# Performance work log

Measured on AMD Instinct MI355X. Metric: run time of the kernel, lower is better.

The kernel has to match this reference:

```python
import jax, jax.numpy as jnp
import numpy as np

B, LQ, D, H, L, P, DFF = 16, 1024, 256, 8, 4, 4, 1024
SHAPES = ((64, 64), (32, 32), (16, 16), (8, 8))  # (H_l, W_l) per level
LV = sum(h * w for h, w in SHAPES)  # 5440
DH = D // H
EPS = 1e-5


def layer_norm(x, g, b):
    m = jnp.mean(x, -1, keepdims=True)
    v = jnp.mean((x - m) ** 2, -1, keepdims=True)
    return (x - m) * jax.lax.rsqrt(v + EPS) * g + b


def mha(q_in, k_in, v_in, w, b, ow, ob):
    # torch nn.MultiheadAttention with packed in_proj [3D, D]
    q = (q_in @ w[:D].T + b[:D]).reshape(B, LQ, H, DH)
    k = (k_in @ w[D:2 * D].T + b[D:2 * D]).reshape(B, LQ, H, DH)
    v = (v_in @ w[2 * D:].T + b[2 * D:]).reshape(B, LQ, H, DH)
    a = jax.nn.softmax(jnp.einsum('bqhd,bkhd->bhqk', q, k) * (1.0 / np.sqrt(DH)), -1)
    o = jnp.einsum('bhqk,bkhd->bqhd', a, v).reshape(B, LQ, D)
    return o @ ow.T + ob


def ms_deform_attn(q, ref, src, value_w, value_b, off_w, off_b, attw_w, attw_b, outp_w, outp_b):
    # value: [B, H, LV, DH]
    value = (src @ value_w.T + value_b).reshape(B, LV, H, DH).transpose(0, 2, 1, 3)
    off = (q @ off_w.T + off_b).reshape(B, LQ, H, L, P, 2)
    attw = jax.nn.softmax((q @ attw_w.T + attw_b).reshape(B, LQ, H, L * P), -1).reshape(B, LQ, H, L, P)
    # offset normalizer = (W_l, H_l) matching (x, y) order of reference points
    normalizer = jnp.array([[w, h] for h, w in SHAPES], jnp.float32)
    loc = ref[:, :, None, :, None, :] + off / normalizer[None, None, None, :, None, :]  # [B,LQ,H,L,P,2]
    out = jnp.zeros((B, LQ, H, DH), jnp.float32)
    start = 0
    for l, (hl, wl) in enumerate(SHAPES):
        v = value[:, :, start:start + hl * wl]  # [B,H,N_l,DH]
        start += hl * wl
        # grid_sample semantics, align_corners=False, padding zeros
        x = loc[:, :, :, l, :, 0] * wl - 0.5  # [B,LQ,H,P]
        y = loc[:, :, :, l, :, 1] * hl - 0.5
        x0 = jnp.floor(x); y0 = jnp.floor(y)
        lx = (x - x0).transpose(0, 2, 1, 3)[..., None]  # [B,H,LQ,P,1]
        ly = (y - y0).transpose(0, 2, 1, 3)[..., None]
        x0i = x0.astype(jnp.int32); y0i = y0.astype(jnp.int32)

        def gather(xi, yi):
            valid = ((xi >= 0) & (xi < wl) & (yi >= 0) & (yi < hl)).astype(jnp.float32)
            idx = jnp.clip(yi, 0, hl - 1) * wl + jnp.clip(xi, 0, wl - 1)  # [B,LQ,H,P]
            idx2 = idx.transpose(0, 2, 1, 3).reshape(B, H, LQ * P)
            g = jnp.take_along_axis(v, jnp.broadcast_to(idx2[..., None], (B, H, LQ * P, DH)), axis=2)
            return g.reshape(B, H, LQ, P, DH) * valid.transpose(0, 2, 1, 3)[..., None]

        g00 = gather(x0i, y0i); g01 = gather(x0i + 1, y0i)
        g10 = gather(x0i, y0i + 1); g11 = gather(x0i + 1, y0i + 1)
        sampled = (g00 * (1 - lx) * (1 - ly) + g01 * lx * (1 - ly)
                   + g10 * (1 - lx) * ly + g11 * lx * ly)  # [B,H,LQ,P,DH]
        out = out + jnp.einsum('bhqpd,bqhp->bqhd', sampled, attw[:, :, :, l])
    return out.reshape(B, LQ, D) @ outp_w.T + outp_b


def setup_inputs() -> dict:
    key = jax.random.key(0)
    ks = jax.random.split(key, 16)
    s = 0.02
    inp = {}
    inp['tgt'] = jax.random.normal(ks[0], (B, LQ, D), jnp.float32)
    inp['query_pos'] = jax.random.normal(ks[1], (B, LQ, D), jnp.float32)
    inp['reference_points'] = jax.random.uniform(ks[2], (B, LQ, L, 2), jnp.float32)
    inp['src'] = jax.random.normal(ks[3], (B, LV, D), jnp.float32)
    # self-attention (MHA)
    inp['in_proj_w'] = jax.random.normal(ks[4], (3 * D, D), jnp.float32) * s
    inp['in_proj_b'] = jnp.zeros((3 * D,), jnp.float32)
    inp['out_proj_w'] = jax.random.normal(ks[5], (D, D), jnp.float32) * s
    inp['out_proj_b'] = jnp.zeros((D,), jnp.float32)
    inp['norm2_g'] = jnp.ones((D,), jnp.float32); inp['norm2_b'] = jnp.zeros((D,), jnp.float32)
    # MSDeformAttn
    inp['value_w'] = jax.random.normal(ks[6], (D, D), jnp.float32) * s
    inp['value_b'] = jnp.zeros((D,), jnp.float32)
    inp['off_w'] = jax.random.normal(ks[7], (H * L * P * 2, D), jnp.float32) * s
    inp['off_b'] = jax.random.normal(ks[8], (H * L * P * 2,), jnp.float32) * 0.5
    inp['attw_w'] = jax.random.normal(ks[9], (H * L * P, D), jnp.float32) * s
    inp['attw_b'] = jnp.zeros((H * L * P,), jnp.float32)
    inp['outp_w'] = jax.random.normal(ks[10], (D, D), jnp.float32) * s
    inp['outp_b'] = jnp.zeros((D,), jnp.float32)
    inp['norm1_g'] = jnp.ones((D,), jnp.float32); inp['norm1_b'] = jnp.zeros((D,), jnp.float32)
    # FFN
    inp['lin1_w'] = jax.random.normal(ks[11], (DFF, D), jnp.float32) * s
    inp['lin1_b'] = jnp.zeros((DFF,), jnp.float32)
    inp['lin2_w'] = jax.random.normal(ks[12], (D, DFF), jnp.float32) * s
    inp['lin2_b'] = jnp.zeros((D,), jnp.float32)
    inp['norm3_g'] = jnp.ones((D,), jnp.float32); inp['norm3_b'] = jnp.zeros((D,), jnp.float32)
    inp['src_spatial_shapes'] = jnp.array(SHAPES, jnp.int32)
    inp['level_start_index'] = jnp.array(np.concatenate([[0], np.cumsum([h * w for h, w in SHAPES[:-1]])]), jnp.int32)
    return inp


def reference(tgt, query_pos, reference_points, src,
              in_proj_w, in_proj_b, out_proj_w, out_proj_b, norm2_g, norm2_b,
              value_w, value_b, off_w, off_b, attw_w, attw_b, outp_w, outp_b,
              norm1_g, norm1_b, lin1_w, lin1_b, lin2_w, lin2_b, norm3_g, norm3_b,
              src_spatial_shapes, level_start_index):
    # dropout=0 (eval mode)
    q = tgt + query_pos
    tgt2 = mha(q, q, tgt, in_proj_w, in_proj_b, out_proj_w, out_proj_b)
    tgt = layer_norm(tgt + tgt2, norm2_g, norm2_b)
    tgt2 = ms_deform_attn(tgt + query_pos, reference_points, src,
                          value_w, value_b, off_w, off_b, attw_w, attw_b, outp_w, outp_b)
    tgt = layer_norm(tgt + tgt2, norm1_g, norm1_b)
    t2 = jax.nn.relu(tgt @ lin1_w.T + lin1_b) @ lin2_w.T + lin2_b
    return layer_norm(tgt + t2, norm3_g, norm3_b)
```

## Files before the change

kernel.cpp:

```cpp
#include <hip/hip_runtime.h>
#include <math.h>

typedef short s16x8 __attribute__((ext_vector_type(8)));
typedef float f32x4 __attribute__((ext_vector_type(4)));
typedef unsigned short u16;
typedef unsigned short u16x4 __attribute__((ext_vector_type(4)));

constexpr int cB    = 16;
constexpr int cLQ   = 1024;
constexpr int cD    = 256;
constexpr int cH    = 8;
constexpr int cLVTOT= 5440;
constexpr int cNTOK = cB * cLQ;
constexpr int cNV   = cB * cLVTOT;

__device__ __forceinline__ u16 f2b(float f) {
    __bf16 h = (__bf16)f;
    u16 u;
    __builtin_memcpy(&u, &h, 2);
    return u;
}
__device__ __forceinline__ float bl(unsigned x) {
    return __uint_as_float(x << 16);
}

__global__ __launch_bounds__(256) void prep_src_kernel(const float4* __restrict__ t,
                                                       const float4* __restrict__ q,
                                                       u16x4* __restrict__ tb,
                                                       u16x4* __restrict__ qb,
                                                       const float4* __restrict__ src,
                                                       u16x4* __restrict__ srcb) {
    int bid = blockIdx.x;
    if (bid < 4096) {
        int i = bid * 256 + threadIdx.x;
        float4 a = t[i], b = q[i];
        tb[i] = (u16x4){ f2b(a.x), f2b(a.y), f2b(a.z), f2b(a.w) };
        qb[i] = (u16x4){ f2b(a.x + b.x), f2b(a.y + b.y), f2b(a.z + b.z), f2b(a.w + b.w) };
    } else {
        int i = (bid - 4096) * 256 + threadIdx.x;
        float4 v = src[i];
        srcb[i] = (u16x4){ f2b(v.x), f2b(v.y), f2b(v.z), f2b(v.w) };
    }
}

struct WArgs { const float4* src[8]; };
__global__ __launch_bounds__(256) void cvtw_kernel(WArgs a, u16x4* __restrict__ out,
                                                   const float* __restrict__ off_b,
                                                   const float* __restrict__ attw_b,
                                                   float* __restrict__ biasoa) {
    int i = blockIdx.x * 256 + threadIdx.x;
    if (i >= 253952) {
        int t = threadIdx.x;
        biasoa[t] = off_b[t];
        if (t < 128) biasoa[256 + t] = attw_b[t];
        return;
    }
    int s, off;
    if (i < 98304) {
        if (i < 65536) { if (i < 49152) { s = 0; off = i; } else { s = 1; off = i - 49152; } }
        else           { if (i < 81920) { s = 2; off = i - 65536; } else { s = 3; off = i - 81920; } }
    } else {
        if (i < 122880){ if (i < 106496){ s = 4; off = i - 98304; } else { s = 5; off = i - 106496; } }
        else           { if (i < 188416){ s = 6; off = i - 122880; } else { s = 7; off = i - 188416; } }
    }
    float4 v = a.src[s][off];
    out[i] = (u16x4){ f2b(v.x), f2b(v.y), f2b(v.z), f2b(v.w) };
}

__global__ __launch_bounds__(256) void gemm_qkv(const u16* __restrict__ A0,
                                                const u16* __restrict__ A1,
                                                const u16* __restrict__ Wt,
                                                const float* __restrict__ bias,
                                                u16* __restrict__ QKb,
                                                u16* __restrict__ Vtg) {
    __shared__ u16 As[128 * 32];
    __shared__ u16 Bs[128 * 32];
    const int K = 256;
    int tid = threadIdx.x;
    int bm = blockIdx.x * 128, bn = blockIdx.y * 128;
    const u16* A = (blockIdx.y < 4) ? A0 : A1;
    int w = tid >> 6, lane = tid & 63, quad = lane >> 4, l15 = lane & 15;
    int wm = (w & 1) * 64, wn = (w >> 1) * 64;
    int r0 = tid >> 2;
    int c0 = ((tid & 3) ^ ((tid >> 3) & 3)) * 8;
    const u16* ga0 = A  + (size_t)(bm + r0) * K + c0;
    const u16* ga1 = ga0 + (size_t)64 * K;
    const u16* gb0 = Wt + (size_t)(bn + r0) * K + c0;
    const u16* gb1 = gb0 + (size_t)64 * K;
    int abk = (quad ^ ((l15 >> 1) & 3)) * 8;
    f32x4 acc[16];
#pragma unroll
    for (int i = 0; i < 16; ++i) acc[i] = (f32x4){0.f, 0.f, 0.f, 0.f};
    s16x8 ra0 = *(const s16x8*)ga0, ra1 = *(const s16x8*)ga1;
    s16x8 rb0 = *(const s16x8*)gb0, rb1 = *(const s16x8*)gb1;
#pragma unroll 2
    for (int i = 0; i < 8; ++i) {
        *(s16x8*)&As[tid * 8]        = ra0;
        *(s16x8*)&As[2048 + tid * 8] = ra1;
        *(s16x8*)&Bs[tid * 8]        = rb0;
        *(s16x8*)&Bs[2048 + tid * 8] = rb1;
        __syncthreads();
        if (i < 7) {
            int k1 = (i + 1) << 5;
            ra0 = *(const s16x8*)(ga0 + k1); ra1 = *(const s16x8*)(ga1 + k1);
            rb0 = *(const s16x8*)(gb0 + k1); rb1 = *(const s16x8*)(gb1 + k1);
        }
        s16x8 af[4], bf[4];
#pragma unroll
        for (int mt = 0; mt < 4; ++mt) af[mt] = *(const s16x8*)&As[(wm + mt * 16 + l15) * 32 + abk];
#pragma unroll
        for (int nt = 0; nt < 4; ++nt) bf[nt] = *(const s16x8*)&Bs[(wn + nt * 16 + l15) * 32 + abk];
#pragma unroll
        for (int mt = 0; mt < 4; ++mt)
#pragma unroll
            for (int nt = 0; nt < 4; ++nt)
                acc[mt * 4 + nt] = __builtin_amdgcn_mfma_f32_16x16x32_bf16(af[mt], bf[nt], acc[mt * 4 + nt], 0, 0, 0);
        __syncthreads();
    }
    float bs[4];
#pragma unroll
    for (int nt = 0; nt < 4; ++nt) bs[nt] = bias[bn + wn + nt * 16 + l15];
    if (bn < 512) {
        float qs = (bn + wn < 256) ? 0.25506734f : 1.0f;
#pragma unroll
        for (int mt = 0; mt < 4; ++mt) {
            int m = bm + wm + mt * 16 + quad * 4;
#pragma unroll
            for (int nt = 0; nt < 4; ++nt) {
                int n = bn + wn + nt * 16 + l15;
#pragma unroll
                for (int r = 0; r < 4; ++r)
                    QKb[(size_t)(m + r) * 512 + n] = f2b((acc[mt * 4 + nt][r] + bs[nt]) * qs);
            }
        }
    } else {
#pragma unroll
        for (int mt = 0; mt < 4; ++mt) {
            int m = bm + wm + mt * 16 + quad * 4;
            int b = m >> 10, t = m & 1023;
#pragma unroll
            for (int nt = 0; nt < 4; ++nt) {
                int nv = bn + wn + nt * 16 + l15 - 512;
                int h = nv >> 5, dh = nv & 31;
                u16x4 o;
#pragma unroll
                for (int r = 0; r < 4; ++r) o[r] = f2b(acc[mt * 4 + nt][r] + bs[nt]);
                *(u16x4*)(Vtg + (((size_t)(b * 8 + h) * 32 + dh) << 10) + t) = o;
            }
        }
    }
}

template <int RELU, int OUTBF>
__global__ __launch_bounds__(256) void gemm128(const u16* __restrict__ A,
                                               const u16* __restrict__ Wt,
                                               const float* __restrict__ bias,
                                               float* __restrict__ Cf,
                                               u16* __restrict__ Cb,
                                               int M, int N, int K) {
    __shared__ u16 As[128 * 32];
    __shared__ u16 Bs[128 * 32];
    int tid = threadIdx.x;
    int bm = blockIdx.x * 128, bn = blockIdx.y * 128;
    int w = tid >> 6, lane = tid & 63, quad = lane >> 4, l15 = lane & 15;
    int wm = (w & 1) * 64, wn = (w >> 1) * 64;
    int r0 = tid >> 2;
    int c0 = ((tid & 3) ^ ((tid >> 3) & 3)) * 8;
    const u16* ga0 = A  + (size_t)(bm + r0) * K + c0;
    const u16* ga1 = ga0 + (size_t)64 * K;
    const u16* gb0 = Wt + (size_t)(bn + r0) * K + c0;
    const u16* gb1 = gb0 + (size_t)64 * K;
    int abk = (quad ^ ((l15 >> 1) & 3)) * 8;
    f32x4 acc[16];
#pragma unroll
    for (int i = 0; i < 16; ++i) acc[i] = (f32x4){0.f, 0.f, 0.f, 0.f};
    s16x8 ra0 = *(const s16x8*)ga0, ra1 = *(const s16x8*)ga1;
    s16x8 rb0 = *(const s16x8*)gb0, rb1 = *(const s16x8*)gb1;
    int nk = K >> 5;
#pragma unroll 2
    for (int i = 0; i < nk; ++i) {
        *(s16x8*)&As[tid * 8]        = ra0;
        *(s16x8*)&As[2048 + tid * 8] = ra1;
        *(s16x8*)&Bs[tid * 8]        = rb0;
        *(s16x8*)&Bs[2048 + tid * 8] = rb1;
        __syncthreads();
        if (i + 1 < nk) {
            int k1 = (i + 1) << 5;
            ra0 = *(const s16x8*)(ga0 + k1); ra1 = *(const s16x8*)(ga1 + k1);
            rb0 = *(const s16x8*)(gb0 + k1); rb1 = *(const s16x8*)(gb1 + k1);
        }
        s16x8 af[4], bf[4];
#pragma unroll
        for (int mt = 0; mt < 4; ++mt) af[mt] = *(const s16x8*)&As[(wm + mt * 16 + l15) * 32 + abk];
#pragma unroll
        for (int nt = 0; nt < 4; ++nt) bf[nt] = *(const s16x8*)&Bs[(wn + nt * 16 + l15) * 32 + abk];
#pragma unroll
        for (int mt = 0; mt < 4; ++mt)
#pragma unroll
            for (int nt = 0; nt < 4; ++nt)
                acc[mt * 4 + nt] = __builtin_amdgcn_mfma_f32_16x16x32_bf16(af[mt], bf[nt], acc[mt * 4 + nt], 0, 0, 0);
        __syncthreads();
    }
    float bs[4];
#pragma unroll
    for (int nt = 0; nt < 4; ++nt) bs[nt] = bias[bn + wn + nt * 16 + l15];
#pragma unroll
    for (int mt = 0; mt < 4; ++mt) {
        int m = bm + wm + mt * 16 + quad * 4;
#pragma unroll
        for (int nt = 0; nt < 4; ++nt) {
            int n = bn + wn + nt * 16 + l15;
#pragma unroll
            for (int r = 0; r < 4; ++r) {
                float v = acc[mt * 4 + nt][r] + bs[nt];
                if (RELU) v = fmaxf(v, 0.f);
                if (OUTBF) Cb[(size_t)(m + r) * N + n] = f2b(v);
                else       Cf[(size_t)(m + r) * N + n] = v;
            }
        }
    }
}

template <int RELU, int OUTBF>
__global__ __launch_bounds__(256) void gemm64(const u16* __restrict__ A,
                                              const u16* __restrict__ Wt,
                                              const float* __restrict__ bias,
                                              float* __restrict__ Cf,
                                              u16* __restrict__ Cb,
                                              int M, int N, int K) {
    __shared__ u16 As[64 * 32];
    __shared__ u16 Bs[128 * 32];
    int tid = threadIdx.x;
    int bm = blockIdx.x * 64, bn = blockIdx.y * 128;
    int w = tid >> 6, lane = tid & 63, quad = lane >> 4, l15 = lane & 15;
    int wn = w * 32;
    int r0 = tid >> 2;
    int c0 = ((tid & 3) ^ ((tid >> 3) & 3)) * 8;
    const u16* ga0 = A  + (size_t)(bm + r0) * K + c0;
    const u16* gb0 = Wt + (size_t)(bn + r0) * K + c0;
    const u16* gb1 = gb0 + (size_t)64 * K;
    int abk = (quad ^ ((l15 >> 1) & 3)) * 8;
    f32x4 acc[8];
#pragma unroll
    for (int i = 0; i < 8; ++i) acc[i] = (f32x4){0.f, 0.f, 0.f, 0.f};
    s16x8 ra0 = *(const s16x8*)ga0;
    s16x8 rb0 = *(const s16x8*)gb0, rb1 = *(const s16x8*)gb1;
    int nk = K >> 5;
#pragma unroll 2
    for (int i = 0; i < nk; ++i) {
        *(s16x8*)&As[tid * 8]        = ra0;
        *(s16x8*)&Bs[tid * 8]        = rb0;
        *(s16x8*)&Bs[2048 + tid * 8] = rb1;
        __syncthreads();
        if (i + 1 < nk) {
            int k1 = (i + 1) << 5;
            ra0 = *(const s16x8*)(ga0 + k1);
            rb0 = *(const s16x8*)(gb0 + k1); rb1 = *(const s16x8*)(gb1 + k1);
        }
        s16x8 af[4], bf[2];
#pragma unroll
        for (int mt = 0; mt < 4; ++mt) af[mt] = *(const s16x8*)&As[(mt * 16 + l15) * 32 + abk];
#pragma unroll
        for (int nt = 0; nt < 2; ++nt) bf[nt] = *(const s16x8*)&Bs[(wn + nt * 16 + l15) * 32 + abk];
#pragma unroll
        for (int mt = 0; mt < 4; ++mt)
#pragma unroll
            for (int nt = 0; nt < 2; ++nt)
                acc[mt * 2 + nt] = __builtin_amdgcn_mfma_f32_16x16x32_bf16(af[mt], bf[nt], acc[mt * 2 + nt], 0, 0, 0);
        __syncthreads();
    }
    float bs[2];
#pragma unroll
    for (int nt = 0; nt < 2; ++nt) bs[nt] = bias[bn + wn + nt * 16 + l15];
#pragma unroll
    for (int mt = 0; mt < 4; ++mt) {
        int m = bm + mt * 16 + quad * 4;
#pragma unroll
        for (int nt = 0; nt < 2; ++nt) {
            int n = bn + wn + nt * 16 + l15;
#pragma unroll
            for (int r = 0; r < 4; ++r) {
                float v = acc[mt * 2 + nt][r] + bs[nt];
                if (RELU) v = fmaxf(v, 0.f);
                if (OUTBF) Cb[(size_t)(m + r) * N + n] = f2b(v);
                else       Cf[(size_t)(m + r) * N + n] = v;
            }
        }
    }
}

__global__ __launch_bounds__(256) void attn_mfma(const u16* __restrict__ QK,
                                                 const u16* __restrict__ Vt,
                                                 u16* __restrict__ O) {
    __shared__ u16 Ks[64 * 40];
    __shared__ u16 Vs[32 * 72];
    __shared__ u16 Ps[4][16 * 72];
    int tid = threadIdx.x, w = tid >> 6, lane = tid & 63, quad = lane >> 4, l15 = lane & 15;
    int qt = blockIdx.x & 15, bh = blockIdx.x >> 4;
    int h = bh & 7, b = bh >> 3;
    int qbase = qt * 64 + w * 16;
    s16x8 qf = *(const s16x8*)(QK + (size_t)(b * cLQ + qbase + l15) * 512 + h * 32 + quad * 8);
    f32x4 o0 = {0.f,0.f,0.f,0.f}, o1 = {0.f,0.f,0.f,0.f};
    float lsum = 0.f;
    int skey = tid >> 2, sdh = (tid & 3) * 8;
    int vdh = tid >> 3, vkc = (tid & 7) * 8;
    size_t kgbase = (size_t)(b * cLQ) * 512 + 256 + h * 32;
    size_t vgbase = (size_t)bh * 32 * cLQ;
    s16x8 kreg = *(const s16x8*)(QK + kgbase + (size_t)skey * 512 + sdh);
    s16x8 vreg = *(const s16x8*)(Vt + vgbase + (size_t)vdh * cLQ + vkc);
    for (int kt = 0; kt < cLQ; kt += 64) {
        __syncthreads();
        *(s16x8*)&Ks[skey * 40 + sdh] = kreg;
        *(s16x8*)&Vs[vdh * 72 + vkc]  = vreg;
        if (kt + 64 < cLQ) {
            kreg = *(const s16x8*)(QK + kgbase + (size_t)(kt + 64 + skey) * 512 + sdh);
            vreg = *(const s16x8*)(Vt + vgbase + (size_t)vdh * cLQ + kt + 64 + vkc);
        }
        __syncthreads();
#pragma unroll
        for (int t = 0; t < 4; ++t) {
            s16x8 kf = *(const s16x8*)&Ks[(t * 16 + l15) * 40 + quad * 8];
            f32x4 z = {0.f,0.f,0.f,0.f};
            f32x4 sc = __builtin_amdgcn_mfma_f32_16x16x32_bf16(kf, qf, z, 0, 0, 0);
            u16x4 pb;
#pragma unroll
            for (int r = 0; r < 4; ++r) {
                float p = exp2f(sc[r]);
                lsum += p;
                pb[r] = f2b(p);
            }
            *(u16x4*)&Ps[w][l15 * 72 + t * 16 + quad * 4] = pb;
        }
#pragma unroll
        for (int ks = 0; ks < 2; ++ks) {
            s16x8 pa  = *(const s16x8*)&Ps[w][l15 * 72 + ks * 32 + quad * 8];
            s16x8 vb0 = *(const s16x8*)&Vs[l15 * 72 + ks * 32 + quad * 8];
            s16x8 vb1 = *(const s16x8*)&Vs[(l15 + 16) * 72 + ks * 32 + quad * 8];
            o0 = __builtin_amdgcn_mfma_f32_16x16x32_bf16(pa, vb0, o0, 0, 0, 0);
            o1 = __builtin_amdgcn_mfma_f32_16x16x32_bf16(pa, vb1, o1, 0, 0, 0);
        }
    }
    lsum += __shfl_xor(lsum, 16);
    lsum += __shfl_xor(lsum, 32);
#pragma unroll
    for (int r = 0; r < 4; ++r) {
        float inv = 1.0f / __shfl(lsum, quad * 4 + r);
        int q = qbase + quad * 4 + r;
        size_t ob = (size_t)(b * cLQ + q) * cD + h * 32;
        O[ob + l15]      = f2b(o0[r] * inv);
        O[ob + 16 + l15] = f2b(o1[r] * inv);
    }
}

template <int WB, int QP>
__global__ __launch_bounds__(256) void add_ln_kernel(const float* __restrict__ X,
                                                     const float* __restrict__ R,
                                                     const float* __restrict__ g,
                                                     const float* __restrict__ bt,
                                                     const float* __restrict__ qp,
                                                     float* __restrict__ out,
                                                     u16* __restrict__ outb) {
    int wave = threadIdx.x / 64;
    int lane = threadIdx.x % 64;
    int row = blockIdx.x * 4 + wave;
    const float* x = X + (size_t)row * cD;
    const float* r = R + (size_t)row * cD;
    float4 xv = *(const float4*)(x + lane * 4);
    float4 rv = *(const float4*)(r + lane * 4);
    float v0 = xv.x + rv.x, v1 = xv.y + rv.y, v2 = xv.z + rv.z, v3 = xv.w + rv.w;
    float s = v0 + v1 + v2 + v3;
    float s2 = v0 * v0 + v1 * v1 + v2 * v2 + v3 * v3;
#pragma unroll
    for (int off = 32; off > 0; off >>= 1) {
        s += __shfl_xor(s, off);
        s2 += __shfl_xor(s2, off);
    }
    float mean = s * (1.0f / 256.0f);
    float var = s2 * (1.0f / 256.0f) - mean * mean;
    float rstd = rsqrtf(var + 1e-5f);
    float4 gv = *(const float4*)(g + lane * 4);
    float4 bv = *(const float4*)(bt + lane * 4);
    float4 o;
    o.x = (v0 - mean) * rstd * gv.x + bv.x;
    o.y = (v1 - mean) * rstd * gv.y + bv.y;
    o.z = (v2 - mean) * rstd * gv.z + bv.z;
    o.w = (v3 - mean) * rstd * gv.w + bv.w;
    *(float4*)(out + (size_t)row * cD + lane * 4) = o;
    if (WB) {
        u16x4 ob = { f2b(o.x), f2b(o.y), f2b(o.z), f2b(o.w) };
        *(u16x4*)(outb + (size_t)row * cD + lane * 4) = ob;
    }
    if (QP) {
        float4 qv = *(const float4*)(qp + (size_t)row * cD + lane * 4);
        u16x4 ob = { f2b(o.x + qv.x), f2b(o.y + qv.y), f2b(o.z + qv.z), f2b(o.w + qv.w) };
        *(u16x4*)(outb + (size_t)row * cD + lane * 4) = ob;
    }
}

__global__ __launch_bounds__(256) void deform_kernel(const u16* __restrict__ value,
                                                     const float* __restrict__ oa,
                                                     const float* __restrict__ refp,
                                                     u16* __restrict__ out) {
    int t = blockIdx.x * 32 + (threadIdx.x >> 3);
    int dq = threadIdx.x & 7;
    int h = t & 7;
    int bq = t >> 3;
    int b = bq >> 10;
    const float* al = oa + (size_t)bq * 384 + 256 + h * 16;
    float wv[16];
    float mx = -1e30f;
#pragma unroll
    for (int i = 0; i < 16; ++i) { wv[i] = al[i]; mx = fmaxf(mx, wv[i]); }
    float sum = 0.f;
#pragma unroll
    for (int i = 0; i < 16; ++i) { wv[i] = __expf(wv[i] - mx); sum += wv[i]; }
    float inv = 1.f / sum;
    const float* off = oa + (size_t)bq * 384 + h * 32;
    const float* rp = refp + (size_t)bq * 8;
    const u16* vb = value + ((size_t)b * cLVTOT) * 256 + h * 32 + dq * 4;
    const int starts[4] = {0, 4096, 5120, 5376};
    const int dims[4] = {64, 32, 16, 8};
    float a0 = 0.f, a1 = 0.f, a2 = 0.f, a3 = 0.f;
#pragma unroll
    for (int l = 0; l < 4; ++l) {
        int hl = dims[l], wl = dims[l];
        float rx = rp[l * 2 + 0], ry = rp[l * 2 + 1];
#pragma unroll
        for (int p = 0; p < 4; ++p) {
            float ox = off[(l * 4 + p) * 2 + 0];
            float oy = off[(l * 4 + p) * 2 + 1];
            float x = rx * (float)wl + ox - 0.5f;
            float y = ry * (float)hl + oy - 0.5f;
            float x0f = floorf(x), y0f = floorf(y);
            float lx = x - x0f, ly = y - y0f;
            int x0 = (int)x0f, y0 = (int)y0f;
            float aw = wv[l * 4 + p] * inv;
            float cw[4] = {(1.f - lx) * (1.f - ly), lx * (1.f - ly),
                           (1.f - lx) * ly, lx * ly};
            int xs[4] = {x0, x0 + 1, x0, x0 + 1};
            int ys[4] = {y0, y0, y0 + 1, y0 + 1};
#pragma unroll
            for (int c = 0; c < 4; ++c) {
                int xi = xs[c], yi = ys[c];
                bool valid = (xi >= 0) && (xi < wl) && (yi >= 0) && (yi < hl);
                int xc = min(max(xi, 0), wl - 1);
                int yc = min(max(yi, 0), hl - 1);
                int idx = starts[l] + yc * wl + xc;
                float wgt = valid ? aw * cw[c] : 0.f;
                unsigned long long u = *(const unsigned long long*)(vb + (size_t)idx * 256);
                a0 += wgt * bl((unsigned)(u & 0xffffull));
                a1 += wgt * bl((unsigned)((u >> 16) & 0xffffull));
                a2 += wgt * bl((unsigned)((u >> 32) & 0xffffull));
                a3 += wgt * bl((unsigned)(u >> 48));
            }
        }
    }
    u16x4 o = { f2b(a0), f2b(a1), f2b(a2), f2b(a3) };
    *(u16x4*)(out + (size_t)bq * 256 + h * 32 + dq * 4) = o;
}

extern "C" void kernel_launch(void* const* d_in, const int* in_sizes, int n_in,
                              void* d_out, int out_size, void* d_ws, size_t ws_size,
                              hipStream_t stream) {
    const float* tgt        = (const float*)d_in[0];
    const float* query_pos  = (const float*)d_in[1];
    const float* refp       = (const float*)d_in[2];
    const float* src        = (const float*)d_in[3];
    const float* in_proj_w  = (const float*)d_in[4];
    const float* in_proj_b  = (const float*)d_in[5];
    const float* out_proj_b = (const float*)d_in[7];
    const float* norm2_g    = (const float*)d_in[8];
    const float* norm2_b    = (const float*)d_in[9];
    const float* value_b    = (const float*)d_in[11];
    const float* off_b      = (const float*)d_in[13];
    const float* attw_b     = (const float*)d_in[15];
    const float* outp_b     = (const float*)d_in[17];
    const float* norm1_g    = (const float*)d_in[18];
    const float* norm1_b    = (const float*)d_in[19];
    const float* lin1_b     = (const float*)d_in[21];
    const float* lin2_b     = (const float*)d_in[23];
    const float* norm3_g    = (const float*)d_in[24];
    const float* norm3_b    = (const float*)d_in[25];

    char* W = (char*)d_ws;
    const size_t S84 = 8388608;
    u16*   tgtb  = (u16*)(W + 0);
    u16*   q2b   = (u16*)(W + 0);
    u16*   qb    = (u16*)(W + 1 * S84);
    u16*   QKb   = (u16*)(W + 2 * S84);
    u16*   dtb   = (u16*)(W + 2 * S84);
    u16*   x2b   = (u16*)(W + 3 * S84);
    float* ffn2f = (float*)(W + 4 * S84);
    u16*   aob   = (u16*)(W + 5 * S84);
    float* oaf   = (float*)(W + 5 * S84);
    u16*   Vtg   = (u16*)(W + 6 * S84);
    float* t2f   = (float*)(W + 6 * S84);
    float* x1f   = (float*)(W + 8 * S84);
    float* x2f   = (float*)(W + 10 * S84);
    u16*   srcb  = (u16*)(W + 12 * S84);
    u16*   ffn1b = (u16*)(W + 12 * S84);
    u16*   valb  = (u16*)(W + 12 * S84 + 44564480);
    char*  wbase = W + 12 * S84 + 2 * 44564480;
    u16* wb_in   = (u16*)(wbase + 0);
    u16* wb_out  = (u16*)(wbase + 393216);
    u16* wb_val  = (u16*)(wbase + 524288);
    u16* wb_off  = (u16*)(wbase + 655360);
    u16* wb_outp = (u16*)(wbase + 851968);
    u16* wb_lin1 = (u16*)(wbase + 983040);
    u16* wb_lin2 = (u16*)(wbase + 1507328);
    float* biasoa= (float*)(wbase + 2031616);
    float* out = (float*)d_out;

    dim3 blk(256);

    prep_src_kernel<<<dim3(25856), blk, 0, stream>>>((const float4*)tgt, (const float4*)query_pos,
                                                     (u16x4*)tgtb, (u16x4*)qb,
                                                     (const float4*)src, (u16x4*)srcb);
    WArgs wa;
    wa.src[0] = (const float4*)in_proj_w;  wa.src[1] = (const float4*)d_in[6];
    wa.src[2] = (const float4*)d_in[10];   wa.src[3] = (const float4*)d_in[12];
    wa.src[4] = (const float4*)d_in[14];   wa.src[5] = (const float4*)d_in[16];
    wa.src[6] = (const float4*)d_in[20];   wa.src[7] = (const float4*)d_in[22];
    cvtw_kernel<<<dim3(993), blk, 0, stream>>>(wa, (u16x4*)wb_in, off_b, attw_b, biasoa);

    gemm_qkv<<<dim3(128, 6), blk, 0, stream>>>(qb, tgtb, wb_in, in_proj_b, QKb, Vtg);
    attn_mfma<<<dim3(cB * cH * 16), blk, 0, stream>>>(QKb, Vtg, aob);
    gemm64<0, 0><<<dim3(256, 2), blk, 0, stream>>>(aob, wb_out, out_proj_b, t2f, nullptr, cNTOK, 256, 256);
    add_ln_kernel<0, 1><<<dim3(4096), blk, 0, stream>>>(tgt, t2f, norm2_g, norm2_b, query_pos, x1f, q2b);

    gemm128<0, 1><<<dim3(680, 2), blk, 0, stream>>>(srcb, wb_val, value_b, nullptr, valb, cNV, 256, 256);
    gemm64<0, 0><<<dim3(256, 3), blk, 0, stream>>>(q2b, wb_off, biasoa, oaf, nullptr, cNTOK, 384, 256);
    deform_kernel<<<dim3(4096), blk, 0, stream>>>(valb, oaf, refp, dtb);
    gemm64<0, 0><<<dim3(256, 2), blk, 0, stream>>>(dtb, wb_outp, outp_b, t2f, nullptr, cNTOK, 256, 256);
    add_ln_kernel<1, 0><<<dim3(4096), blk, 0, stream>>>(x1f, t2f, norm1_g, norm1_b, nullptr, x2f, x2b);

    gemm128<1, 1><<<dim3(128, 8), blk, 0, stream>>>(x2b, wb_lin1, lin1_b, nullptr, ffn1b, cNTOK, 1024, 256);
    gemm64<0, 0><<<dim3(256, 2), blk, 0, stream>>>(ffn1b, wb_lin2, lin2_b, ffn2f, nullptr, cNTOK, 256, 1024);
    add_ln_kernel<0, 0><<<dim3(4096), blk, 0, stream>>>(x2f, ffn2f, norm3_g, norm3_b, nullptr, out, nullptr);
}
```

Baseline: 443.2 us.

## Co-schedule value projection GEMM with self-attention in one interleaved launch

```diff
diff --git a/kernel.cpp b/kernel.cpp
--- a/kernel.cpp
+++ b/kernel.cpp
@@ -289,29 +289,102 @@
     }
 }
 
-__global__ __launch_bounds__(256) void attn_mfma(const u16* __restrict__ QK,
-                                                 const u16* __restrict__ Vt,
-                                                 u16* __restrict__ O) {
-    __shared__ u16 Ks[64 * 40];
-    __shared__ u16 Vs[32 * 72];
-    __shared__ u16 Ps[4][16 * 72];
-    int tid = threadIdx.x, w = tid >> 6, lane = tid & 63, quad = lane >> 4, l15 = lane & 15;
-    int qt = blockIdx.x & 15, bh = blockIdx.x >> 4;
+__global__ __launch_bounds__(256) void attn_val(const u16* __restrict__ QK,
+                                                const u16* __restrict__ Vt,
+                                                u16* __restrict__ O,
+                                                const u16* __restrict__ Av,
+                                                const u16* __restrict__ Wv,
+                                                const float* __restrict__ bv,
+                                                u16* __restrict__ Cv) {
+    __shared__ __align__(16) u16 smem[8192];
+    int bid = blockIdx.x;
+    int tid = threadIdx.x;
+    int w = tid >> 6, lane = tid & 63, quad = lane >> 4, l15 = lane & 15;
+    int isg, id;
+    if (bid < 2720) { isg = !(bid & 1); id = bid >> 1; }
+    else            { isg = 0;          id = 1360 + (bid - 2720); }
+    if (isg) {
+        u16* As = smem;
+        u16* Bs = smem + 4096;
+        int bm = (id % 680) * 128, bn = (id / 680) * 128;
+        int wm = (w & 1) * 64, wn = (w >> 1) * 64;
+        int r0 = tid >> 2;
+        int c0 = ((tid & 3) ^ ((tid >> 3) & 3)) * 8;
+        const u16* ga0 = Av + (size_t)(bm + r0) * 256 + c0;
+        const u16* ga1 = ga0 + (size_t)64 * 256;
+        const u16* gb0 = Wv + (size_t)(bn + r0) * 256 + c0;
+        const u16* gb1 = gb0 + (size_t)64 * 256;
+        int abk = (quad ^ ((l15 >> 1) & 3)) * 8;
+        f32x4 acc[16];
+#pragma unroll
+        for (int i = 0; i < 16; ++i) acc[i] = (f32x4){0.f, 0.f, 0.f, 0.f};
+        s16x8 ra0 = *(const s16x8*)ga0, ra1 = *(const s16x8*)ga1;
+        s16x8 rb0 = *(const s16x8*)gb0, rb1 = *(const s16x8*)gb1;
+#pragma unroll 2
+        for (int i = 0; i < 8; ++i) {
+            *(s16x8*)&As[tid * 8]        = ra0;
+            *(s16x8*)&As[2048 + tid * 8] = ra1;
+            *(s16x8*)&Bs[tid * 8]        = rb0;
+            *(s16x8*)&Bs[2048 + tid * 8] = rb1;
+            __syncthreads();
+            if (i < 7) {
+                int k1 = (i + 1) << 5;
+                ra0 = *(const s16x8*)(ga0 + k1); ra1 = *(const s16x8*)(ga1 + k1);
+                rb0 = *(const s16x8*)(gb0 + k1); rb1 = *(const s16x8*)(gb1 + k1);
+            }
+            s16x8 af[4], bf[4];
+#pragma unroll
+            for (int mt = 0; mt < 4; ++mt) af[mt] = *(const s16x8*)&As[(wm + mt * 16 + l15) * 32 + abk];
+#pragma unroll
+            for (int nt = 0; nt < 4; ++nt) bf[nt] = *(const s16x8*)&Bs[(wn + nt * 16 + l15) * 32 + abk];
+#pragma unroll
+            for (int mt = 0; mt < 4; ++mt)
+#pragma unroll
+                for (int nt = 0; nt < 4; ++nt)
+                    acc[mt * 4 + nt] = __builtin_amdgcn_mfma_f32_16x16x32_bf16(af[mt], bf[nt], acc[mt * 4 + nt], 0, 0, 0);
+            __syncthreads();
+        }
+        float bs[4];
+#pragma unroll
+        for (int nt = 0; nt < 4; ++nt) bs[nt] = bv[bn + wn + nt * 16 + l15];
+#pragma unroll
+        for (int mt = 0; mt < 4; ++mt) {
+            int m = bm + wm + mt * 16 + quad * 4;
+#pragma unroll
+            for (int nt = 0; nt < 4; ++nt) {
+                int n = bn + wn + nt * 16 + l15;
+#pragma unroll
+                for (int r = 0; r < 4; ++r)
+                    Cv[(size_t)(m + r) * 256 + n] = f2b(acc[mt * 4 + nt][r] + bs[nt]);
+            }
+        }
+        return;
+    }
+    u16* Ks  = smem;
+    u16* Vs  = smem + 2048;
+    u16* Psw = smem + 4096 + w * 1024;
+    int qt = id & 15, bh = id >> 4;
     int h = bh & 7, b = bh >> 3;
     int qbase = qt * 64 + w * 16;
     s16x8 qf = *(const s16x8*)(QK + (size_t)(b * cLQ + qbase + l15) * 512 + h * 32 + quad * 8);
-    f32x4 o0 = {0.f,0.f,0.f,0.f}, o1 = {0.f,0.f,0.f,0.f};
-    float lsum = 0.f;
-    int skey = tid >> 2, sdh = (tid & 3) * 8;
-    int vdh = tid >> 3, vkc = (tid & 7) * 8;
+    f32x4 o0 = {0.f,0.f,0.f,0.f}, o1 = {0.f,0.f,0.f,0.f}, o2 = {0.f,0.f,0.f,0.f};
+    int skey = tid >> 2, kchunk = tid & 3;
+    int ks_off = skey * 32 + ((kchunk ^ ((skey >> 1) & 3)) * 8);
+    int sdh = kchunk * 8;
+    int vdh = tid >> 3, vchunk = tid & 7;
+    int vs_off = vdh * 64 + ((vchunk ^ (vdh & 7)) * 8);
+    int vkc = vchunk * 8;
+    int ksw = (l15 >> 1) & 3;
+    int vsw = l15 & 7;
     size_t kgbase = (size_t)(b * cLQ) * 512 + 256 + h * 32;
     size_t vgbase = (size_t)bh * 32 * cLQ;
     s16x8 kreg = *(const s16x8*)(QK + kgbase + (size_t)skey * 512 + sdh);
     s16x8 vreg = *(const s16x8*)(Vt + vgbase + (size_t)vdh * cLQ + vkc);
+    const s16x8 ones = {16256,16256,16256,16256,16256,16256,16256,16256};
     for (int kt = 0; kt < cLQ; kt += 64) {
         __syncthreads();
-        *(s16x8*)&Ks[skey * 40 + sdh] = kreg;
-        *(s16x8*)&Vs[vdh * 72 + vkc]  = vreg;
+        *(s16x8*)&Ks[ks_off] = kreg;
+        *(s16x8*)&Vs[vs_off] = vreg;
         if (kt + 64 < cLQ) {
             kreg = *(const s16x8*)(QK + kgbase + (size_t)(kt + 64 + skey) * 512 + sdh);
             vreg = *(const s16x8*)(Vt + vgbase + (size_t)vdh * cLQ + kt + 64 + vkc);
@@ -319,32 +392,28 @@
         __syncthreads();
 #pragma unroll
         for (int t = 0; t < 4; ++t) {
-            s16x8 kf = *(const s16x8*)&Ks[(t * 16 + l15) * 40 + quad * 8];
+            s16x8 kf = *(const s16x8*)&Ks[(t * 16 + l15) * 32 + (quad ^ ksw) * 8];
             f32x4 z = {0.f,0.f,0.f,0.f};
             f32x4 sc = __builtin_amdgcn_mfma_f32_16x16x32_bf16(kf, qf, z, 0, 0, 0);
             u16x4 pb;
 #pragma unroll
-            for (int r = 0; r < 4; ++r) {
-                float p = exp2f(sc[r]);
-                lsum += p;
-                pb[r] = f2b(p);
-            }
-            *(u16x4*)&Ps[w][l15 * 72 + t * 16 + quad * 4] = pb;
+            for (int r = 0; r < 4; ++r) pb[r] = f2b(exp2f(sc[r]));
+            *(u16x4*)&Psw[l15 * 64 + (((t * 2 + (quad >> 1)) ^ vsw) * 8) + (quad & 1) * 4] = pb;
         }
 #pragma unroll
         for (int ks = 0; ks < 2; ++ks) {
-            s16x8 pa  = *(const s16x8*)&Ps[w][l15 * 72 + ks * 32 + quad * 8];
-            s16x8 vb0 = *(const s16x8*)&Vs[l15 * 72 + ks * 32 + quad * 8];
-            s16x8 vb1 = *(const s16x8*)&Vs[(l15 + 16) * 72 + ks * 32 + quad * 8];
+            int coff = ((ks * 4 + quad) ^ vsw) * 8;
+            s16x8 pa  = *(const s16x8*)&Psw[l15 * 64 + coff];
+            s16x8 vb0 = *(const s16x8*)&Vs[l15 * 64 + coff];
+            s16x8 vb1 = *(const s16x8*)&Vs[(l15 + 16) * 64 + coff];
             o0 = __builtin_amdgcn_mfma_f32_16x16x32_bf16(pa, vb0, o0, 0, 0, 0);
             o1 = __builtin_amdgcn_mfma_f32_16x16x32_bf16(pa, vb1, o1, 0, 0, 0);
-        }
-    }
-    lsum += __shfl_xor(lsum, 16);
-    lsum += __shfl_xor(lsum, 32);
+            o2 = __builtin_amdgcn_mfma_f32_16x16x32_bf16(pa, ones, o2, 0, 0, 0);
+        }
+    }
 #pragma unroll
     for (int r = 0; r < 4; ++r) {
-        float inv = 1.0f / __shfl(lsum, quad * 4 + r);
+        float inv = 1.0f / o2[r];
         int q = qbase + quad * 4 + r;
         size_t ob = (size_t)(b * cLQ + q) * cD + h * 32;
         O[ob + l15]      = f2b(o0[r] * inv);
@@ -524,11 +593,10 @@
     cvtw_kernel<<<dim3(993), blk, 0, stream>>>(wa, (u16x4*)wb_in, off_b, attw_b, biasoa);
 
     gemm_qkv<<<dim3(128, 6), blk, 0, stream>>>(qb, tgtb, wb_in, in_proj_b, QKb, Vtg);
-    attn_mfma<<<dim3(cB * cH * 16), blk, 0, stream>>>(QKb, Vtg, aob);
+    attn_val<<<dim3(3408), blk, 0, stream>>>(QKb, Vtg, aob, srcb, wb_val, value_b, valb);
     gemm64<0, 0><<<dim3(256, 2), blk, 0, stream>>>(aob, wb_out, out_proj_b, t2f, nullptr, cNTOK, 256, 256);
     add_ln_kernel<0, 1><<<dim3(4096), blk, 0, stream>>>(tgt, t2f, norm2_g, norm2_b, query_pos, x1f, q2b);
 
-    gemm128<0, 1><<<dim3(680, 2), blk, 0, stream>>>(srcb, wb_val, value_b, nullptr, valb, cNV, 256, 256);
     gemm64<0, 0><<<dim3(256, 3), blk, 0, stream>>>(q2b, wb_off, biasoa, oaf, nullptr, cNTOK, 384, 256);
     deform_kernel<<<dim3(4096), blk, 0, stream>>>(valb, oaf, refp, dtb);
     gemm64<0, 0><<<dim3(256, 2), blk, 0, stream>>>(dtb, wb_outp, outp_b, t2f, nullptr, cNTOK, 256, 256);
```

Result: no change. 440.3 us (-0.6%).
